# Performance work log

Measured on AMD Instinct MI355X. Metric: run time of the kernel, lower is better.

Reference implementation:

```python
import jax, jax.numpy as jnp
import numpy as np

EPS_BN = 1e-5
K_DET = 50

def conv2d(x, w, b, pad):
    y = jax.lax.conv_general_dilated(x, w, (1, 1), [(pad, pad), (pad, pad)],
                                     dimension_numbers=('NCHW', 'OIHW', 'NCHW'))
    return y + b[None, :, None, None]

def branch2(x, w1, b1, w2, b2):
    # conv3x3 -> relu -> conv1x1
    return conv2d(jax.nn.relu(conv2d(x, w1, b1, 1)), w2, b2, 0)

def roi_head(x, w1, b1, g, beta, m, v, w2, b2):
    # conv3x3 -> BN(eval) -> relu -> global avg pool -> conv1x1
    h = conv2d(x, w1, b1, 1)
    h = (h - m[None, :, None, None]) * (g[None, :, None, None] / jnp.sqrt(v[None, :, None, None] + EPS_BN)) + beta[None, :, None, None]
    h = jax.nn.relu(h)
    h = jnp.mean(h, axis=(2, 3), keepdims=True)
    return conv2d(h, w2, b2, 0)[:, :, 0, 0]

def nms_hm(heat, kernel=3):
    pad = (kernel - 1) // 2
    hmax = jax.lax.reduce_window(heat, -jnp.inf, jax.lax.max,
                                 (1, 1, kernel, kernel), (1, 1, 1, 1),
                                 [(0, 0), (0, 0), (pad, pad), (pad, pad)])
    return heat * (hmax == heat).astype(heat.dtype)

def select_topk(heat, K):
    B, C, H, W = heat.shape
    s_all, i_all = jax.lax.top_k(heat.reshape(B, C, H * W), K)   # per-class topk
    scores, idx = jax.lax.top_k(s_all.reshape(B, C * K), K)      # overall topk
    classes = idx // K
    inds = jnp.take_along_axis(i_all.reshape(B, C * K), idx, axis=1)  # flat HW inds
    return scores, inds, classes

def roi_align_7x7(feat, boxes, sr=2):
    # torchvision roi_align, spatial_scale=1, aligned=False, sampling_ratio=sr
    B, C, H, W = feat.shape
    N = boxes.shape[0]
    b = boxes[:, 0].astype(jnp.int32)
    x1, y1, x2, y2 = boxes[:, 1], boxes[:, 2], boxes[:, 3], boxes[:, 4]
    roi_w = jnp.maximum(x2 - x1, 1.0)
    roi_h = jnp.maximum(y2 - y1, 1.0)
    bw = roi_w / 7.0
    bh = roi_h / 7.0
    S = 7 * sr
    off = (jnp.arange(S, dtype=feat.dtype) + 0.5) / sr  # sample offsets in bin units
    xs = x1[:, None] + bw[:, None] * off[None, :]       # (N,S)
    ys = y1[:, None] + bh[:, None] * off[None, :]
    X = jnp.broadcast_to(xs[:, None, :], (N, S, S))
    Y = jnp.broadcast_to(ys[:, :, None], (N, S, S))
    valid = (X > -1.0) & (X < W) & (Y > -1.0) & (Y < H)
    Xc = jnp.clip(X, 0.0, W - 1.0)
    Yc = jnp.clip(Y, 0.0, H - 1.0)
    x0 = jnp.floor(Xc).astype(jnp.int32)
    y0 = jnp.floor(Yc).astype(jnp.int32)
    x1i = jnp.minimum(x0 + 1, W - 1)
    y1i = jnp.minimum(y0 + 1, H - 1)
    lx = Xc - x0
    ly = Yc - y0
    flat = feat.transpose(0, 2, 3, 1).reshape(B * H * W, C)
    base = (b * H * W)[:, None, None]
    g = lambda yy, xx: flat[base + yy * W + xx]  # (N,S,S,C)
    v = (((1 - ly) * (1 - lx))[..., None] * g(y0, x0)
         + ((1 - ly) * lx)[..., None] * g(y0, x1i)
         + (ly * (1 - lx))[..., None] * g(y1i, x0)
         + (ly * lx)[..., None] * g(y1i, x1i))
    v = v * valid[..., None]
    v = v.reshape(N, 7, sr, 7, sr, C).mean(axis=(2, 4))
    return v.transpose(0, 3, 1, 2)  # (N,C,7,7)

def project_to_rect(calib, pts):
    c_u, c_v = calib[:, 0, 2], calib[:, 1, 2]
    f_u, f_v = calib[:, 0, 0], calib[:, 1, 1]
    b_x = calib[:, 0, 3] / (-f_u)
    b_y = calib[:, 1, 3] / (-f_v)
    x = (pts[:, 0] - c_u) * pts[:, 2] / f_u + b_x
    y = (pts[:, 1] - c_v) * pts[:, 2] / f_v + b_y
    return jnp.stack([x, y, pts[:, 2]], -1)

HEAD_NAMES = ['dep', 'o3', 's3', 'hd']

def setup_inputs():
    key = jax.random.key(0)
    ks = iter(jax.random.split(key, 64))
    B, Cin, H, W = 8, 64, 96, 320
    HC, NC = 256, 3
    f32 = jnp.float32
    rn = lambda shape, s=0.02: s * jax.random.normal(next(ks), shape, f32)
    inp = {}
    inp['features'] = jax.random.normal(next(ks), (B, Cin, H, W), f32)
    base = jnp.array([[700., 0., 640., 0.], [0., 700., 192., 0.], [0., 0., 1., 0.]], f32)
    inp['calib'] = base[None] + (jax.random.uniform(next(ks), (B, 3, 4), f32) - 0.5) * 2.0
    crb = jnp.array([[0., 0.], [1280., 384.]], f32)
    inp['coord_ranges'] = crb[None] + (jax.random.uniform(next(ks), (B, 2, 2), f32) - 0.5) * 2.0
    inp['mean_size'] = jnp.array([[3.88, 1.63, 1.53], [0.84, 0.66, 1.76], [1.76, 0.60, 1.73]], f32)
    inp['hm_w1'] = rn((HC, Cin, 3, 3)); inp['hm_b1'] = jnp.zeros(HC, f32)
    inp['hm_w2'] = rn((3, HC, 1, 1)); inp['hm_b2'] = jnp.full((3,), -np.log(1 / 0.1 - 1), f32)
    inp['o2_w1'] = rn((HC, Cin, 3, 3)); inp['o2_b1'] = jnp.zeros(HC, f32)
    inp['o2_w2'] = rn((2, HC, 1, 1)); inp['o2_b2'] = jnp.zeros(2, f32)
    inp['s2_w1'] = rn((HC, Cin, 3, 3)); inp['s2_b1'] = jnp.zeros(HC, f32)
    inp['s2_w2'] = rn((2, HC, 1, 1)); inp['s2_b2'] = 8.0 * jnp.ones(2, f32)
    Croi = Cin + 2 + NC
    for name, oc in zip(HEAD_NAMES, [2, 2, 4, 24]):
        inp[name + '_w1'] = rn((HC, Croi, 3, 3)); inp[name + '_b1'] = jnp.zeros(HC, f32)
        inp[name + '_g'] = 1.0 + 0.1 * jax.random.normal(next(ks), (HC,), f32)
        inp[name + '_beta'] = 0.1 * jax.random.normal(next(ks), (HC,), f32)
        inp[name + '_m'] = 0.1 * jax.random.normal(next(ks), (HC,), f32)
        inp[name + '_v'] = 1.0 + jax.random.uniform(next(ks), (HC,), f32)
        inp[name + '_w2'] = rn((oc, HC, 1, 1)); inp[name + '_b2'] = jnp.zeros(oc, f32)
    return inp

def reference(features, calib, coord_ranges, mean_size,
              hm_w1, hm_b1, hm_w2, hm_b2,
              o2_w1, o2_b1, o2_w2, o2_b2,
              s2_w1, s2_b1, s2_w2, s2_b2,
              dep_w1, dep_b1, dep_g, dep_beta, dep_m, dep_v, dep_w2, dep_b2,
              o3_w1, o3_b1, o3_g, o3_beta, o3_m, o3_v, o3_w2, o3_b2,
              s3_w1, s3_b1, s3_g, s3_beta, s3_m, s3_v, s3_w2, s3_b2,
              hd_w1, hd_b1, hd_g, hd_beta, hd_m, hd_v, hd_w2, hd_b2):
    B, Cf, H, W = features.shape
    dt = features.dtype
    heatmap = branch2(features, hm_w1, hm_b1, hm_w2, hm_b2)    # (B,3,H,W)
    offset_2d = branch2(features, o2_w1, o2_b1, o2_w2, o2_b2)  # (B,2,H,W)
    size_2d = branch2(features, s2_w1, s2_b1, s2_w2, s2_b2)    # (B,2,H,W)
    heat = nms_hm(heatmap)
    _, inds, classes = select_topk(heat, K_DET)                # (B,K)
    # coord map and box2d maps (B,5,H,W): [batch_idx, x1,y1,x2,y2]
    xs = jnp.arange(W, dtype=dt)
    ys = jnp.arange(H, dtype=dt)
    coord = jnp.stack([jnp.broadcast_to(xs[None, :], (H, W)),
                       jnp.broadcast_to(ys[:, None], (H, W))], 0)[None]
    center = coord + offset_2d
    bidx = jnp.broadcast_to(jnp.arange(B, dtype=dt)[:, None, None, None], (B, 1, H, W))
    box2d_maps = jnp.concatenate([bidx, center - size_2d / 2, center + size_2d / 2], 1)
    bm = box2d_maps.reshape(B, 5, H * W).transpose(0, 2, 1)    # (B,HW,5)
    boxes = jnp.take_along_axis(bm, inds[:, :, None], axis=1).reshape(-1, 5)  # (N,5)
    N = boxes.shape[0]
    roi_feat = roi_align_7x7(features, boxes)                  # (N,C,7,7)
    rb = boxes[:, 0].astype(jnp.int32)
    cr = coord_ranges[rb]                                      # (N,2,2)
    sx = cr[:, 1, 0] - cr[:, 0, 0]
    sy = cr[:, 1, 1] - cr[:, 0, 1]
    box_img = jnp.stack([boxes[:, 0],
                         boxes[:, 1] / W * sx + cr[:, 0, 0],
                         boxes[:, 2] / H * sy + cr[:, 0, 1],
                         boxes[:, 3] / W * sx + cr[:, 0, 0],
                         boxes[:, 4] / H * sy + cr[:, 0, 1]], -1)
    roi_calib = calib[rb]                                      # (N,3,4)
    ones = jnp.ones((N, 1), dt)
    p1 = project_to_rect(roi_calib, jnp.concatenate([box_img[:, 1:3], ones], -1))[:, :2]
    p2 = project_to_rect(roi_calib, jnp.concatenate([box_img[:, 3:5], ones], -1))[:, :2]
    t = jnp.arange(7, dtype=dt) / 6.0
    cx = p1[:, 0:1] + t[None, :] * (p2[:, 0:1] - p1[:, 0:1])   # (N,7)
    cy = p1[:, 1:2] + t[None, :] * (p2[:, 1:2] - p1[:, 1:2])
    coord_maps = jnp.stack([jnp.broadcast_to(cx[:, None, :], (N, 7, 7)),
                            jnp.broadcast_to(cy[:, :, None], (N, 7, 7))], 1)
    cls = classes.reshape(-1)
    NC = mean_size.shape[0]
    cls_hot = jax.nn.one_hot(cls, NC, dtype=dt)
    roi_in = jnp.concatenate([roi_feat, coord_maps,
                              jnp.broadcast_to(cls_hot[:, :, None, None], (N, NC, 7, 7))], 1)
    box2d_h = jnp.maximum(box_img[:, 4] - box_img[:, 2], 1.0)
    s3 = roi_head(roi_in, s3_w1, s3_b1, s3_g, s3_beta, s3_m, s3_v, s3_w2, s3_b2)  # (N,4)
    h3d_log_std = s3[:, 3:4]
    size3d_offset = s3[:, :3]
    size_3d = mean_size[cls] + size3d_offset
    f_u = roi_calib[:, 0, 0]
    depth_geo = size_3d[:, 0] / box2d_h * f_u
    dep = roi_head(roi_in, dep_w1, dep_b1, dep_g, dep_beta, dep_m, dep_v, dep_w2, dep_b2)
    depth_geo_log_std = (h3d_log_std[:, 0] + 2.0 * (jnp.log(f_u) - jnp.log(box2d_h)))[:, None]
    depth_log_std = jax.nn.logsumexp(jnp.concatenate([dep[:, 1:2], depth_geo_log_std], -1), axis=-1, keepdims=True)
    depth = jnp.concatenate([1.0 / (jax.nn.sigmoid(dep[:, 0:1]) + 1e-6) - 1.0 + depth_geo[:, None],
                             depth_log_std], -1)
    heading = roi_head(roi_in, hd_w1, hd_b1, hd_g, hd_beta, hd_m, hd_v, hd_w2, hd_b2)
    offset_3d = roi_head(roi_in, o3_w1, o3_b1, o3_g, o3_beta, o3_m, o3_v, o3_w2, o3_b2)
    return (heatmap, offset_2d, size_2d, heading, depth, offset_3d, size3d_offset, h3d_log_std)
```

## Files before the change

kernel.cpp:

```cpp
#include <hip/hip_runtime.h>
#include <math.h>

typedef unsigned short u16;
typedef unsigned int   u32;
typedef unsigned long long u64;
typedef __attribute__((ext_vector_type(8))) short short8;
typedef __attribute__((ext_vector_type(4))) float f32x4;

__device__ __forceinline__ float b2f(u16 v) { return __uint_as_float(((u32)v) << 16); }
__device__ __forceinline__ u16 f2b(float f) {
    u32 u = __float_as_uint(f);
    u32 r = (u + 0x7FFFu + ((u >> 16) & 1u)) >> 16;
    return (u16)r;
}
__device__ __forceinline__ float gload(const void* p, long i, int bf) {
    return bf ? b2f(((const u16*)p)[i]) : ((const float*)p)[i];
}
__device__ __forceinline__ void gstore(void* p, long i, float v, int bf) {
    if (bf) ((u16*)p)[i] = f2b(v);
    else    ((float*)p)[i] = v;
}

__device__ __forceinline__ u64 packKey(float v, int idx) {
    u32 u = __float_as_uint(v);
    u32 m = (u & 0x80000000u) ? ~u : (u | 0x80000000u);
    return ((u64)(~m) << 32) | (u32)idx;
}

__device__ int blockFlag(const void* feat) {
    __shared__ int fcnt;
    if (threadIdx.x == 0) fcnt = 0;
    __syncthreads();
    int sane = 0;
    for (int i = threadIdx.x; i < 512; i += blockDim.x) {
        u16 v = ((const u16*)feat)[i];
        float f = b2f(v);
        u32 e = (v >> 7) & 0xFF;
        float a = fabsf(f);
        sane += (e != 0xFF) && (f == 0.f || (a >= 1e-8f && a <= 1e4f));
    }
    atomicAdd(&fcnt, sane);
    __syncthreads();
    return fcnt >= 480;
}

#define BATCH 8
#define CIN   64
#define FH    96
#define FW    320
#define KDET  50
#define NROI  400
#define CROI  69
#define HW    (FH*FW)
#define CHUNK 1920
#define NCHUNK 16

#define WS_HEAT 0L
#define WS_OFF2 737280L
#define WS_SIZ2 1228800L
#define WS_NH   1720320L
#define WS_CLS  2460000L
#define WS_BOX  2460400L
#define WS_ROI  2462400L
#define WS_HOUT 3814800L
#define WS_W1T  3827600L
#define WS_WB16 3975056L
#define WS_W1H  4269968L
#define WS_PAR  4905872L
#define WS_FLAG 4938960L
#define WS_FEATT 4938964L
#define WS_END  (WS_FEATT + 7864320L)

#define PB_CAL 0
#define PB_CRN 96
#define PB_MSZ 128
#define PB_BR0 144
#define PB_HD0 3264

#define O_HEAT 0L
#define O_OFF2 737280L
#define O_SIZ2 1228800L
#define O_HEAD 1720320L
#define O_DEP  1729920L
#define O_OFF3 1730720L
#define O_S3D  1731520L
#define O_H3D  1732720L

struct WPtrs { const void* bw[3]; const void* hw[4]; };
struct Seg { const void* src; int n; int dst; };
struct Segs { Seg s[40]; int cnt; };

__global__ void kPrepWP(WPtrs P, Segs S, const void* __restrict__ feat,
                        int* __restrict__ flag, float* __restrict__ w1t,
                        u16* __restrict__ wb16, u16* __restrict__ whb,
                        float* __restrict__ par) {
    const int bf = blockFlag(feat);
    if (blockIdx.x == 0 && threadIdx.x == 0) *flag = bf;
    if (blockIdx.x < 5760) {
        int idx = blockIdx.x * 256 + threadIdx.x;
        if (idx < 147456) {
            int k = idx >> 8, c = idx & 255;
            w1t[idx] = gload(P.bw[0], (long)c * 576 + k, bf);
        } else if (idx < 589824) {
            int j = idx - 147456;
            int br = j / 147456, rem = j % 147456;
            int tap = rem / 16384;
            int r2 = rem & 16383;
            int s = r2 >> 13;
            int n = (r2 >> 5) & 255;
            int c5 = r2 & 31;
            int ci = s * 32 + c5;
            wb16[j] = f2b(gload(P.bw[br], (long)n * 576 + ci * 9 + tap, bf));
        } else {
            int j = idx - 589824;
            int h = j / 221184, rem = j % 221184;
            int tap = rem / 24576, rem2 = rem % 24576;
            int cs = rem2 / 8192, rem3 = rem2 % 8192;
            int oc = rem3 >> 5, jj = rem3 & 31;
            int ci = cs * 32 + jj;
            u16 val = 0;
            if (ci < CROI) val = f2b(gload(P.hw[h], (long)oc * 621 + ci * 9 + tap, bf));
            whb[j] = val;
        }
    } else {
        int sidx = blockIdx.x - 5760;
        if (sidx < S.cnt) {
            Seg sg = S.s[sidx];
            for (int i = threadIdx.x; i < sg.n; i += 256)
                par[sg.dst + i] = gload(sg.src, i, bf);
        }
    }
}

union MLds {
    struct { u16 a[4][68][72]; float red[8][64][3]; } c;
    struct {
        float in[4][3][36];
        union { float w[36 * 256]; float part[32 * 3 * 32]; } u;
    } s;
    u16 t[64][72];
};

__global__ __launch_bounds__(512, 4)
void kBranch3M(const void* __restrict__ feat, const int* __restrict__ flag,
               const u16* __restrict__ wbAll,
               const float* __restrict__ bpAll,
               const float* __restrict__ w1t,
               void* __restrict__ outb, float* __restrict__ wsbase) {
    __shared__ __align__(16) MLds L;

    const long obase[3] = {O_HEAT, O_OFF2, O_SIZ2};
    const long wfs[3]   = {WS_HEAT, WS_OFF2, WS_SIZ2};

    const int bfl = *flag;
    const int tid = threadIdx.x;

    if (blockIdx.z == 9) {
        u16* featT = (u16*)(wsbase + WS_FEATT);
        const int x0 = blockIdx.x * 64;
        const int y0 = blockIdx.y * 2;
        for (int sub = 0; sub < 16; ++sub) {
            const int b = sub >> 1, y = y0 + (sub & 1);
            __syncthreads();
            for (int i = tid; i < 64 * 64; i += 512) {
                int c = i >> 6, x = i & 63;
                L.t[x][c] = f2b(gload(feat, ((long)(b * CIN + c) * FH + y) * FW + x0 + x, bfl));
            }
            __syncthreads();
            u16* outp = featT + (((long)b * FH + y) * FW + x0) * 64;
            for (int i = tid; i < 64 * 64; i += 512) {
                int x = i >> 6, c = i & 63;
                outp[(long)x * 64 + c] = L.t[x][c];
            }
        }
        return;
    }

    if (blockIdx.z == 8) {
        const int sidx = blockIdx.y * 5 + blockIdx.x;
        const int x0 = (sidx % 10) * 32;
        const int srem = sidx / 10;
        const int y = srem % 3;
        const int b = srem / 3;
        const float* bp = bpAll;
        const int OC = 3;
        const int xg = tid & 7, cg = tid >> 3;
        const int c0 = (cg & 31) * 8;

        float acc[8][4];
#pragma unroll
        for (int i = 0; i < 8; ++i)
#pragma unroll
            for (int j = 0; j < 4; ++j) acc[i][j] = 0.f;

        for (int chunk = 0; chunk < 16; ++chunk) {
            const int ci0 = chunk * 4;
            __syncthreads();
            for (int i = tid; i < 4 * 3 * 36; i += 512) {
                int xx = i % 36, t2 = i / 36;
                int r = t2 % 3, ci = t2 / 3;
                int gx = x0 - 1 + xx, gy = y - 1 + r;
                float v = 0.f;
                if (gx >= 0 && gx < FW && gy >= 0 && gy < FH)
                    v = gload(feat, ((long)(b * CIN + ci0 + ci) * FH + gy) * FW + gx, bfl);
                L.s.in[ci][r][xx] = v;
            }
            {
                const float4* src = (const float4*)(w1t + (long)ci0 * 9 * 256);
                float4* dst = (float4*)L.s.u.w;
                for (int i = tid; i < 36 * 256 / 4; i += 512) dst[i] = src[i];
            }
            __syncthreads();
            if (tid < 256) {
#pragma unroll
                for (int ci = 0; ci < 4; ++ci) {
#pragma unroll
                    for (int ky = 0; ky < 3; ++ky) {
                        const float* rowp = &L.s.in[ci][ky][xg * 4];
                        float inv[6];
                        *(float4*)&inv[0] = *(const float4*)&rowp[0];
                        *(float2*)&inv[4] = *(const float2*)&rowp[4];
#pragma unroll
                        for (int kx = 0; kx < 3; ++kx) {
                            const float* wp = &L.s.u.w[(ci * 9 + ky * 3 + kx) * 256 + c0];
                            float wv[8];
                            *(float4*)&wv[0] = *(const float4*)&wp[0];
                            *(float4*)&wv[4] = *(const float4*)&wp[4];
#pragma unroll
                            for (int cc = 0; cc < 8; ++cc)
#pragma unroll
                                for (int xx = 0; xx < 4; ++xx)
                                    acc[cc][xx] = fmaf(wv[cc], inv[xx + kx], acc[cc][xx]);
                        }
                    }
                }
            }
        }

        if (tid < 256) {
#pragma unroll
            for (int cc = 0; cc < 8; ++cc) {
                float b1v = bp[c0 + cc];
#pragma unroll
                for (int xx = 0; xx < 4; ++xx)
                    acc[cc][xx] = fmaxf(acc[cc][xx] + b1v, 0.f);
            }
        }
        __syncthreads();
        if (tid < 256) {
#pragma unroll
            for (int k = 0; k < OC; ++k) {
                float p[4];
#pragma unroll
                for (int xx = 0; xx < 4; ++xx) p[xx] = 0.f;
#pragma unroll
                for (int cc = 0; cc < 8; ++cc) {
                    float wv = bp[256 + k * 256 + c0 + cc];
#pragma unroll
                    for (int xx = 0; xx < 4; ++xx) p[xx] = fmaf(acc[cc][xx], wv, p[xx]);
                }
#pragma unroll
                for (int xx = 0; xx < 4; ++xx)
                    L.s.u.part[((cg & 31) * OC + k) * 32 + xg * 4 + xx] = p[xx];
            }
        }
        __syncthreads();
        float* outf = wsbase + WS_HEAT;
        for (int t = tid; t < OC * 32; t += 512) {
            int k = t >> 5, xx = t & 31;
            float s = bp[256 + OC * 256 + k];
#pragma unroll 8
            for (int g = 0; g < 32; ++g) s += L.s.u.part[(g * OC + k) * 32 + xx];
            long o = (((long)b * OC + k) * FH + y) * FW + x0 + xx;
            gstore(outb, O_HEAT + o, s, bfl);
            outf[o] = s;
        }
        return;
    }

    const int wave = tid >> 6, lane = tid & 63;
    const int q = lane >> 4, n15 = lane & 15;
    const int mg = wave >> 2, ng = wave & 3;
    const int x0 = blockIdx.x * 64, y0 = blockIdx.y * 2;
    const int b = blockIdx.z;

    if (tid < 256) {
        const int ci = tid & 63, rr = tid >> 6;
        const int gy = y0 - 1 + rr;
        if (gy < 0 || gy >= FH) {
            for (int xi = 0; xi < 66; ++xi) L.c.a[rr][xi][ci] = 0;
        } else if (bfl) {
            const u16* rp = (const u16*)feat + ((long)((b << 6) | ci) * FH + gy) * FW;
            for (int j = 0; j < 10; ++j) {
                int xs0 = x0 - 8 + j * 8;
                u16 tmp[8];
                if (xs0 >= 0 && xs0 <= FW - 8)
                    *(uint4*)tmp = *(const uint4*)(rp + xs0);
                else
                    for (int e = 0; e < 8; ++e) {
                        int gx = xs0 + e;
                        tmp[e] = (gx >= 0 && gx < FW) ? rp[gx] : (u16)0;
                    }
                for (int e = 0; e < 8; ++e) {
                    int xi = xs0 + e - x0 + 1;
                    if (xi >= 0 && xi < 66) L.c.a[rr][xi][ci] = tmp[e];
                }
            }
        } else {
            const float* rp = (const float*)feat + ((long)((b << 6) | ci) * FH + gy) * FW;
            for (int j = 0; j < 18; ++j) {
                int xs0 = x0 - 4 + j * 4;
                float tmp[4];
                if (xs0 >= 0 && xs0 <= FW - 4)
                    *(float4*)tmp = *(const float4*)(rp + xs0);
                else
                    for (int e = 0; e < 4; ++e) {
                        int gx = xs0 + e;
                        tmp[e] = (gx >= 0 && gx < FW) ? rp[gx] : 0.f;
                    }
                for (int e = 0; e < 4; ++e) {
                    int xi = xs0 + e - x0 + 1;
                    if (xi >= 0 && xi < 66) L.c.a[rr][xi][ci] = f2b(tmp[e]);
                }
            }
        }
    }
    __syncthreads();

#pragma unroll 1
    for (int br = 0; br < 3; ++br) {
        const int oc = (br == 0) ? 3 : 2;
        const u16* wpt = wbAll + br * 147456;
        const float* bp = bpAll + br * 1040;

        f32x4 acc[4][4];
#pragma unroll
        for (int i = 0; i < 4; ++i)
#pragma unroll
            for (int t = 0; t < 4; ++t) acc[i][t] = (f32x4){0.f, 0.f, 0.f, 0.f};

#pragma unroll 1
        for (int tap = 0; tap < 9; ++tap) {
            const int ky = tap / 3, kx = tap % 3;
#pragma unroll
            for (int s = 0; s < 2; ++s) {
                const u16* wks = wpt + (tap * 2 + s) * 8192;
                short8 bfr[4];
#pragma unroll
                for (int t = 0; t < 4; ++t)
                    bfr[t] = *(const short8*)(wks + (ng * 64 + t * 16 + n15) * 32 + q * 8);
                short8 afr[4];
#pragma unroll
                for (int i = 0; i < 4; ++i)
                    afr[i] = *(const short8*)&L.c.a[mg + ky][i * 16 + n15 + kx][s * 32 + q * 8];
#pragma unroll
                for (int i = 0; i < 4; ++i)
#pragma unroll
                    for (int t = 0; t < 4; ++t)
                        acc[i][t] = __builtin_amdgcn_mfma_f32_16x16x32_bf16(
                            afr[i], bfr[t], acc[i][t], 0, 0, 0);
            }
        }

        float b1v[4], w2v[3][4];
#pragma unroll
        for (int t = 0; t < 4; ++t) {
            int n = ng * 64 + t * 16 + n15;
            b1v[t] = bp[n];
#pragma unroll
            for (int k = 0; k < 3; ++k) w2v[k][t] = bp[256 + k * 256 + n];
        }
        __syncthreads();
#pragma unroll
        for (int i = 0; i < 4; ++i) {
#pragma unroll
            for (int r = 0; r < 4; ++r) {
                float pk[3];
#pragma unroll
                for (int k = 0; k < 3; ++k) pk[k] = 0.f;
#pragma unroll
                for (int t = 0; t < 4; ++t) {
                    float h = fmaxf(acc[i][t][r] + b1v[t], 0.f);
#pragma unroll
                    for (int k = 0; k < 3; ++k) pk[k] = fmaf(h, w2v[k][t], pk[k]);
                }
#pragma unroll
                for (int k = 0; k < 3; ++k) {
                    pk[k] += __shfl_xor(pk[k], 1);
                    pk[k] += __shfl_xor(pk[k], 2);
                    pk[k] += __shfl_xor(pk[k], 4);
                    pk[k] += __shfl_xor(pk[k], 8);
                }
                if (n15 == 0) {
                    int ml = i * 16 + q * 4 + r;
#pragma unroll
                    for (int k = 0; k < 3; ++k) L.c.red[wave][ml][k] = pk[k];
                }
            }
        }
        __syncthreads();
        float* outf = wsbase + wfs[br];
        for (int t2 = tid; t2 < oc * 128; t2 += 512) {
            int k = t2 >> 7, m = t2 & 127;
            int row = m >> 6, x = m & 63;
            int mg2 = m >> 6, ml = m & 63;
            float s = bp[256 + oc * 256 + k];
#pragma unroll
            for (int w = 0; w < 4; ++w) s += L.c.red[mg2 * 4 + w][ml][k];
            int grow = y0 + row;
            if (br == 0 && grow < 3) continue;
            long o = (((long)b * oc + k) * FH + grow) * FW + x0 + x;
            gstore(outb, obase[br] + o, s, bfl);
            outf[o] = s;
        }
    }
}

__global__ __launch_bounds__(256)
void kNmsTopA(const float* __restrict__ heat, float* __restrict__ nh) {
    __shared__ float hrow[8][320];
    __shared__ u64 keys[CHUNK];
    __shared__ u64 sub[4][KDET];
    const int bc = blockIdx.x, ch = blockIdx.y;
    const int tid = threadIdx.x;
    const int wave = tid >> 6, lane = tid & 63;
    const int r0 = ch * 6;
    const float* hp = heat + (long)bc * HW;

    for (int i = tid; i < 8 * 320; i += 256) {
        int rr = i / 320, x = i % 320;
        int gy = r0 - 1 + rr;
        hrow[rr][x] = (gy >= 0 && gy < FH) ? hp[(long)gy * FW + x] : -INFINITY;
    }
    __syncthreads();
    for (int i = tid; i < CHUNK; i += 256) {
        int ry = i / 320, x = i % 320;
        float v = hrow[ry + 1][x];
        float m = v;
        int xm = max(x - 1, 0), xp = min(x + 1, FW - 1);
#pragma unroll
        for (int dy = 0; dy < 3; ++dy) {
            m = fmaxf(m, hrow[ry + dy][xm]);
            m = fmaxf(m, hrow[ry + dy][x]);
            m = fmaxf(m, hrow[ry + dy][xp]);
        }
        float nv = (v == m) ? v : 0.f;
        keys[i] = packKey(nv, ch * CHUNK + i);
    }
    __syncthreads();
    {
        u64* kw = keys + wave * 480;
        for (int it = 0; it < KDET; ++it) {
            u64 bk = ~0ULL; int bp = 0;
            for (int i = lane; i < 480; i += 64) {
                u64 k = kw[i];
                if (k < bk) { bk = k; bp = i; }
            }
#pragma unroll
            for (int s = 32; s > 0; s >>= 1) {
                u64 k2 = __shfl_down(bk, s);
                int p2 = __shfl_down(bp, s);
                if (k2 < bk) { bk = k2; bp = p2; }
            }
            bk = __shfl(bk, 0);
            bp = __shfl(bp, 0);
            if (lane == 0) {
                sub[wave][it] = bk;
                kw[bp] = ~0ULL;
            }
        }
    }
    __syncthreads();
    if (wave == 0) {
        u64* outp = (u64*)(nh + (long)bc * HW + (long)ch * CHUNK);
        u64* sp = &sub[0][0];
        for (int it = 0; it < KDET; ++it) {
            u64 bk = ~0ULL; int bp = 0;
            for (int i = lane; i < 4 * KDET; i += 64) {
                u64 k = sp[i];
                if (k < bk) { bk = k; bp = i; }
            }
#pragma unroll
            for (int s = 32; s > 0; s >>= 1) {
                u64 k2 = __shfl_down(bk, s);
                int p2 = __shfl_down(bp, s);
                if (k2 < bk) { bk = k2; bp = p2; }
            }
            bk = __shfl(bk, 0);
            bp = __shfl(bp, 0);
            if (lane == 0) {
                outp[it] = bk;
                sp[bp] = ~0ULL;
            }
        }
    }
}

__global__ __launch_bounds__(192)
void kTopBC(const float* __restrict__ nh, const float* __restrict__ off2,
            const float* __restrict__ siz2, float* __restrict__ boxes,
            int* __restrict__ clsArr) {
    __shared__ u64 keys[3][NCHUNK * KDET];
    __shared__ float sc[150];
    __shared__ int   si[150];
    const int b = blockIdx.x, tid = threadIdx.x;
    const int wave = tid >> 6, lane = tid & 63;
    const int bc = b * 3 + wave;

    for (int ch = 0; ch < NCHUNK; ++ch) {
        const u64* src = (const u64*)(nh + (long)bc * HW + (long)ch * CHUNK);
        if (lane < KDET) keys[wave][ch * KDET + lane] = src[lane];
    }
    __syncthreads();
    for (int it = 0; it < KDET; ++it) {
        u64 bk = ~0ULL; int bp = 0;
        for (int i = lane; i < NCHUNK * KDET; i += 64) {
            u64 k = keys[wave][i];
            if (k < bk) { bk = k; bp = i; }
        }
#pragma unroll
        for (int s = 32; s > 0; s >>= 1) {
            u64 k2 = __shfl_down(bk, s);
            int p2 = __shfl_down(bp, s);
            if (k2 < bk) { bk = k2; bp = p2; }
        }
        bk = __shfl(bk, 0);
        bp = __shfl(bp, 0);
        if (lane == 0) {
            u32 hm = ~(u32)(bk >> 32);
            u32 u = (hm & 0x80000000u) ? (hm & 0x7fffffffu) : ~hm;
            sc[wave * KDET + it] = __uint_as_float(u);
            si[wave * KDET + it] = (int)(bk & 0xFFFFFFFFu);
            keys[wave][bp] = ~0ULL;
        }
    }
    __syncthreads();
    if (wave == 0) {
        const int t = lane;
        for (int r = 0; r < KDET; ++r) {
            float bv = -INFINITY; int bp = 0x7fffffff;
            for (int i = t; i < 150; i += 64) {
                float v = sc[i];
                if (v > bv) { bv = v; bp = i; }
            }
#pragma unroll
            for (int s = 32; s > 0; s >>= 1) {
                float v2 = __shfl_down(bv, s);
                int   p2 = __shfl_down(bp, s);
                if (v2 > bv || (v2 == bv && p2 < bp)) { bv = v2; bp = p2; }
            }
            bp = __shfl(bp, 0);
            if (t == 0) {
                int cls = bp / KDET;
                int ind = si[bp];
                int n = b * KDET + r;
                clsArr[n] = cls;
                int x = ind % FW, yy = ind / FW;
                float cx = (float)x  + off2[(((long)b * 2 + 0) * FH + yy) * FW + x];
                float cy = (float)yy + off2[(((long)b * 2 + 1) * FH + yy) * FW + x];
                float w  = siz2[(((long)b * 2 + 0) * FH + yy) * FW + x];
                float h  = siz2[(((long)b * 2 + 1) * FH + yy) * FW + x];
                boxes[n * 5 + 0] = (float)b;
                boxes[n * 5 + 1] = cx - w * 0.5f;
                boxes[n * 5 + 2] = cy - h * 0.5f;
                boxes[n * 5 + 3] = cx + w * 0.5f;
                boxes[n * 5 + 4] = cy + h * 0.5f;
                sc[bp] = -INFINITY;
            }
// ... 234 lines not shown

    int oyA[4], oxA[4];
#pragma unroll
    for (int i = 0; i < 4; ++i) {
        int pos = i * 16 + n15; if (pos > 48) pos = 48;
        oyA[i] = pos / 7; oxA[i] = pos % 7;
    }

    f32x4 acc[4][4];
#pragma unroll
    for (int i = 0; i < 4; ++i)
#pragma unroll
        for (int t = 0; t < 4; ++t) acc[i][t] = (f32x4){0.f, 0.f, 0.f, 0.f};

#pragma unroll 1
    for (int tap = 0; tap < 9; ++tap) {
        const int ky = tap / 3, kx = tap % 3;
        const u16* wt = whb + ((long)h * 9 + tap) * 24576;
#pragma unroll
        for (int cs = 0; cs < 3; ++cs) {
            short8 afr[4], bfr[4];
#pragma unroll
            for (int i = 0; i < 4; ++i)
                afr[i] = *(const short8*)&r_lds[oyA[i] + ky][oxA[i] + kx][cs * 32 + q * 8];
#pragma unroll
            for (int t = 0; t < 4; ++t)
                bfr[t] = *(const short8*)(wt + ((cs << 8) + wave * 64 + t * 16 + n15) * 32 + q * 8);
#pragma unroll
            for (int i = 0; i < 4; ++i)
#pragma unroll
                for (int t = 0; t < 4; ++t)
                    acc[i][t] = __builtin_amdgcn_mfma_f32_16x16x32_bf16(
                        afr[i], bfr[t], acc[i][t], 0, 0, 0);
        }
    }

    const float* hb = par + PB_HD0 + h * 7456;
#pragma unroll
    for (int t = 0; t < 4; ++t) {
        int oc = wave * 64 + t * 16 + n15;
        float b1 = hb[oc], g = hb[256 + oc], be = hb[512 + oc];
        float m = hb[768 + oc], v = hb[1024 + oc];
        float scale = g / sqrtf(v + 1e-5f);
        float s = 0.f;
#pragma unroll
        for (int i = 0; i < 4; ++i)
#pragma unroll
            for (int r = 0; r < 4; ++r) {
                int pos = i * 16 + q * 4 + r;
                if (pos < 49)
                    s += fmaxf((acc[i][t][r] + b1 - m) * scale + be, 0.f);
            }
        s += __shfl_xor(s, 16);
        s += __shfl_xor(s, 32);
        if (q == 0) means[oc] = s / 49.f;
    }
    __syncthreads();

    int oc_out = ocArr[h];
    const float* w2 = hb + 1280;
    for (int k = wave; k < oc_out; k += 4) {
        float s = 0.f;
        for (int c = lane; c < 256; c += 64) s += means[c] * w2[k * 256 + c];
#pragma unroll
        for (int off = 32; off > 0; off >>= 1) s += __shfl_down(s, off);
        if (lane == 0)
            head_out[(long)n * 32 + offArr[h] + k] = s + w2[oc_out * 256 + k];
    }
}

__global__ void kFinal(const float* __restrict__ head_out, const float* __restrict__ boxes,
                       const int* __restrict__ clsArr, const float* __restrict__ par,
                       void* __restrict__ out, const int* __restrict__ flag) {
    int n = blockIdx.x * 256 + threadIdx.x;
    if (n >= NROI) return;
    const int bf = *flag;
    const float* ho = head_out + (long)n * 32;
    float dep0 = ho[0], dep1 = ho[1];
    int b = (int)boxes[n * 5 + 0];
    int cls = clsArr[n];

    for (int j = 0; j < 24; ++j) gstore(out, O_HEAD + n * 24 + j, ho[8 + j], bf);
    gstore(out, O_OFF3 + n * 2 + 0, ho[2], bf);
    gstore(out, O_OFF3 + n * 2 + 1, ho[3], bf);
    gstore(out, O_S3D + n * 3 + 0, ho[4], bf);
    gstore(out, O_S3D + n * 3 + 1, ho[5], bf);
    gstore(out, O_S3D + n * 3 + 2, ho[6], bf);
    gstore(out, O_H3D + n, ho[7], bf);

    float cry0 = par[PB_CRN + b * 4 + 1], cry1 = par[PB_CRN + b * 4 + 3];
    float sy = cry1 - cry0;
    float bi2 = boxes[n * 5 + 2] / (float)FH * sy + cry0;
    float bi4 = boxes[n * 5 + 4] / (float)FH * sy + cry0;
    float box_h = fmaxf(bi4 - bi2, 1.f);
    float f_u = par[PB_CAL + b * 12 + 0];
    float size3d0 = par[PB_MSZ + cls * 3 + 0] + ho[4];
    float depth_geo = size3d0 / box_h * f_u;
    float sig = 1.f / (1.f + expf(-dep0));
    float d0 = 1.f / (sig + 1e-6f) - 1.f + depth_geo;
    float dgls = ho[7] + 2.f * (logf(f_u) - logf(box_h));
    float mx = fmaxf(dep1, dgls);
    float lse = mx + logf(expf(dep1 - mx) + expf(dgls - mx));
    gstore(out, O_DEP + n * 2 + 0, d0, bf);
    gstore(out, O_DEP + n * 2 + 1, lse, bf);
}

extern "C" void kernel_launch(void* const* d_in, const int* in_sizes, int n_in,
                              void* d_out, int out_size, void* d_ws, size_t ws_size,
                              hipStream_t stream) {
    (void)in_sizes; (void)n_in; (void)out_size;
    float* ws = (float*)d_ws;
    float* par = ws + WS_PAR;
    int* flag = (int*)(ws + WS_FLAG);
    u16* wb16 = (u16*)(ws + WS_WB16);
    u16* whb  = (u16*)(ws + WS_W1H);
    u16* featT = (u16*)(ws + WS_FEATT);
    const void* feat = d_in[0];
    const bool bigws = ws_size >= (size_t)WS_END * 4;

    WPtrs WP;
    WP.bw[0] = d_in[4]; WP.bw[1] = d_in[8]; WP.bw[2] = d_in[12];
    WP.hw[0] = d_in[16]; WP.hw[1] = d_in[24]; WP.hw[2] = d_in[32]; WP.hw[3] = d_in[40];

    Segs SG; int si = 0;
    auto add = [&](const void* s, int n, int dst) {
        SG.s[si].src = s; SG.s[si].n = n; SG.s[si].dst = dst; ++si;
    };
    add(d_in[1], 96, PB_CAL); add(d_in[2], 32, PB_CRN); add(d_in[3], 9, PB_MSZ);
    const int ocb[3] = {3, 2, 2};
    for (int b = 0; b < 3; ++b) {
        int base = PB_BR0 + b * 1040;
        int i0 = 4 + 4 * b;
        add(d_in[i0 + 1], 256, base);
        add(d_in[i0 + 2], ocb[b] * 256, base + 256);
        add(d_in[i0 + 3], ocb[b], base + 256 + ocb[b] * 256);
    }
    const int och[4] = {2, 2, 4, 24};
    for (int h = 0; h < 4; ++h) {
        int base = PB_HD0 + h * 7456;
        int i0 = 16 + 8 * h;
        add(d_in[i0 + 1], 256, base);
        add(d_in[i0 + 2], 256, base + 256);
        add(d_in[i0 + 3], 256, base + 512);
        add(d_in[i0 + 4], 256, base + 768);
        add(d_in[i0 + 5], 256, base + 1024);
        add(d_in[i0 + 6], och[h] * 256, base + 1280);
        add(d_in[i0 + 7], och[h], base + 1280 + och[h] * 256);
    }
    SG.cnt = si;

    kPrepWP<<<5760 + 40, 256, 0, stream>>>(WP, SG, feat, flag,
                                           ws + WS_W1T, wb16, whb, par);

    kBranch3M<<<dim3(5, 48, bigws ? 10 : 9), 512, 0, stream>>>(
        feat, flag, wb16, par + PB_BR0, ws + WS_W1T, d_out, ws);

    kNmsTopA<<<dim3(24, NCHUNK), 256, 0, stream>>>(ws + WS_HEAT, ws + WS_NH);
    kTopBC<<<8, 192, 0, stream>>>(ws + WS_NH, ws + WS_OFF2, ws + WS_SIZ2,
                                  ws + WS_BOX, (int*)(ws + WS_CLS));
    if (bigws) {
        kHeadM2<<<dim3(4, NROI), 256, 0, stream>>>(featT, ws + WS_BOX,
                                                   (int*)(ws + WS_CLS), whb, par,
                                                   ws + WS_HOUT);
    } else {
        kRoi<<<400, 256, 0, stream>>>(feat, flag, ws + WS_BOX, (int*)(ws + WS_CLS),
                                      par, ws + WS_ROI);
        kHeadM<<<dim3(4, NROI), 256, 0, stream>>>(ws + WS_ROI, whb, par, ws + WS_HOUT);
    }
    kFinal<<<2, 256, 0, stream>>>(ws + WS_HOUT, ws + WS_BOX, (int*)(ws + WS_CLS),
                                  par, d_out, flag);
}
```

Before: 745.2 us.

## Fuse feature transpose into conv tile load and software-pipeline MFMA loop

The separate transpose blocks (z==9), which re-read the feature map, are removed. Instead, each conv block writes its already-staged bf16 LDS tile out to the NHWC featT buffer. The per-branch MFMA loop is split into two output-channel halves with 4x2 accumulators and double-buffered A/B fragment loads across taps, which lowers register pressure and overlaps loads with MFMAs. The reduction buffer is double-buffered by branch, which removes one barrier per branch. The risk is extra A-fragment LDS reads, since each half reloads A, plus the added epilogue passes.

```diff
diff --git a/kernel.cpp b/kernel.cpp
--- a/kernel.cpp
+++ b/kernel.cpp
@@ -133,12 +133,11 @@
 }
 
 union MLds {
-    struct { u16 a[4][68][72]; float red[8][64][3]; } c;
+    struct { u16 a[4][68][72]; float red[2][8][64][3]; } c;
     struct {
         float in[4][3][36];
         union { float w[36 * 256]; float part[32 * 3 * 32]; } u;
     } s;
-    u16 t[64][72];
 };
 
 __global__ __launch_bounds__(512, 4)
@@ -146,7 +145,7 @@
                const u16* __restrict__ wbAll,
                const float* __restrict__ bpAll,
                const float* __restrict__ w1t,
-               void* __restrict__ outb, float* __restrict__ wsbase) {
+               void* __restrict__ outb, float* __restrict__ wsbase, int doT) {
     __shared__ __align__(16) MLds L;
 
     const long obase[3] = {O_HEAT, O_OFF2, O_SIZ2};
@@ -155,28 +154,7 @@
     const int bfl = *flag;
     const int tid = threadIdx.x;
 
-    if (blockIdx.z == 9) {
-        u16* featT = (u16*)(wsbase + WS_FEATT);
-        const int x0 = blockIdx.x * 64;
-        const int y0 = blockIdx.y * 2;
-        for (int sub = 0; sub < 16; ++sub) {
-            const int b = sub >> 1, y = y0 + (sub & 1);
-            __syncthreads();
-            for (int i = tid; i < 64 * 64; i += 512) {
-                int c = i >> 6, x = i & 63;
-                L.t[x][c] = f2b(gload(feat, ((long)(b * CIN + c) * FH + y) * FW + x0 + x, bfl));
-            }
-            __syncthreads();
-            u16* outp = featT + (((long)b * FH + y) * FW + x0) * 64;
-            for (int i = tid; i < 64 * 64; i += 512) {
-                int x = i >> 6, c = i & 63;
-                outp[(long)x * 64 + c] = L.t[x][c];
-            }
-        }
-        return;
-    }
-
-    if (blockIdx.z == 8) {
+    if (blockIdx.z == 0) {
         const int sidx = blockIdx.y * 5 + blockIdx.x;
         const int x0 = (sidx % 10) * 32;
         const int srem = sidx / 10;
@@ -282,7 +260,7 @@
     const int q = lane >> 4, n15 = lane & 15;
     const int mg = wave >> 2, ng = wave & 3;
     const int x0 = blockIdx.x * 64, y0 = blockIdx.y * 2;
-    const int b = blockIdx.z;
+    const int b = blockIdx.z - 1;
 
     if (tid < 256) {
         const int ci = tid & 63, rr = tid >> 6;
@@ -327,77 +305,108 @@
     }
     __syncthreads();
 
+    if (doT) {
+        u16* featT = (u16*)(wsbase + WS_FEATT);
+        for (int i = tid; i < 1024; i += 512) {
+            int c8 = i & 7, x = (i >> 3) & 63, r = i >> 9;
+            uint4 v = *(const uint4*)&L.c.a[1 + r][1 + x][c8 * 8];
+            *(uint4*)(featT + (((long)b * FH + y0 + r) * FW + x0 + x) * 64 + c8 * 8) = v;
+        }
+    }
+
+    const u16* aflat = &L.c.a[0][0][0];
+    const int wlane = (ng * 64 + n15) * 32 + q * 8;
+    const int abase = mg * 4896 + n15 * 72 + q * 8;
+
+#define LOADB2(k, dst) { \
+    const u16* wk_ = wph + (k) * 8192; \
+    dst[0] = *(const short8*)(wk_); \
+    dst[1] = *(const short8*)(wk_ + 512); }
+#define LOADA4(k, dst) { \
+    const int tap_ = (k) >> 1, s_ = (k) & 1; \
+    const int ky_ = tap_ / 3, kx_ = tap_ - 3 * ky_; \
+    const u16* ap_ = aflat + abase + ky_ * 4896 + kx_ * 72 + s_ * 32; \
+    dst[0] = *(const short8*)(ap_); \
+    dst[1] = *(const short8*)(ap_ + 1152); \
+    dst[2] = *(const short8*)(ap_ + 2304); \
+    dst[3] = *(const short8*)(ap_ + 3456); }
+#define MFMA42(afr, bfr) { \
+    _Pragma("unroll") \
+    for (int i_ = 0; i_ < 4; ++i_) { \
+        _Pragma("unroll") \
+        for (int t_ = 0; t_ < 2; ++t_) \
+            acc[i_][t_] = __builtin_amdgcn_mfma_f32_16x16x32_bf16( \
+                afr[i_], bfr[t_], acc[i_][t_], 0, 0, 0); } }
+
 #pragma unroll 1
     for (int br = 0; br < 3; ++br) {
         const int oc = (br == 0) ? 3 : 2;
         const u16* wpt = wbAll + br * 147456;
         const float* bp = bpAll + br * 1040;
-
-        f32x4 acc[4][4];
-#pragma unroll
-        for (int i = 0; i < 4; ++i)
-#pragma unroll
-            for (int t = 0; t < 4; ++t) acc[i][t] = (f32x4){0.f, 0.f, 0.f, 0.f};
+        float (*redb)[64][3] = L.c.red[br & 1];
 
 #pragma unroll 1
-        for (int tap = 0; tap < 9; ++tap) {
-            const int ky = tap / 3, kx = tap % 3;
-#pragma unroll
-            for (int s = 0; s < 2; ++s) {
-                const u16* wks = wpt + (tap * 2 + s) * 8192;
-                short8 bfr[4];
-#pragma unroll
-                for (int t = 0; t < 4; ++t)
-                    bfr[t] = *(const short8*)(wks + (ng * 64 + t * 16 + n15) * 32 + q * 8);
-                short8 afr[4];
-#pragma unroll
-                for (int i = 0; i < 4; ++i)
-                    afr[i] = *(const short8*)&L.c.a[mg + ky][i * 16 + n15 + kx][s * 32 + q * 8];
-#pragma unroll
-                for (int i = 0; i < 4; ++i)
-#pragma unroll
-                    for (int t = 0; t < 4; ++t)
-                        acc[i][t] = __builtin_amdgcn_mfma_f32_16x16x32_bf16(
-                            afr[i], bfr[t], acc[i][t], 0, 0, 0);
-            }
-        }
-
-        float b1v[4], w2v[3][4];
-#pragma unroll
-        for (int t = 0; t < 4; ++t) {
-            int n = ng * 64 + t * 16 + n15;
-            b1v[t] = bp[n];
-#pragma unroll
-            for (int k = 0; k < 3; ++k) w2v[k][t] = bp[256 + k * 256 + n];
-        }
-        __syncthreads();
-#pragma unroll
-        for (int i = 0; i < 4; ++i) {
-#pragma unroll
-            for (int r = 0; r < 4; ++r) {
-                float pk[3];
-#pragma unroll
-                for (int k = 0; k < 3; ++k) pk[k] = 0.f;
-#pragma unroll
-                for (int t = 0; t < 4; ++t) {
-                    float h = fmaxf(acc[i][t][r] + b1v[t], 0.f);
-#pragma unroll
-                    for (int k = 0; k < 3; ++k) pk[k] = fmaf(h, w2v[k][t], pk[k]);
+        for (int hf = 0; hf < 2; ++hf) {
+            const u16* wph = wpt + wlane + hf * 1024;
+
+            f32x4 acc[4][2];
+#pragma unroll
+            for (int i = 0; i < 4; ++i)
+#pragma unroll
+                for (int t = 0; t < 2; ++t) acc[i][t] = (f32x4){0.f, 0.f, 0.f, 0.f};
+
+            short8 aA[4], aB[4], bA[2], bB[2];
+            LOADB2(0, bA);
+            LOADA4(0, aA);
+#pragma unroll 1
+            for (int st = 0; st < 18; st += 2) {
+                LOADB2(st + 1, bB);
+                LOADA4(st + 1, aB);
+                MFMA42(aA, bA);
+                if (st + 2 < 18) { LOADB2(st + 2, bA); LOADA4(st + 2, aA); }
+                MFMA42(aB, bB);
+            }
+
+            float b1v[2], w2v[3][2];
+#pragma unroll
+            for (int t = 0; t < 2; ++t) {
+                int n = ng * 64 + (hf * 2 + t) * 16 + n15;
+                b1v[t] = bp[n];
+#pragma unroll
+                for (int k = 0; k < 3; ++k) w2v[k][t] = bp[256 + k * 256 + n];
+            }
+#pragma unroll
+            for (int i = 0; i < 4; ++i) {
+#pragma unroll
+                for (int r = 0; r < 4; ++r) {
+                    float pk[3] = {0.f, 0.f, 0.f};
+#pragma unroll
+                    for (int t = 0; t < 2; ++t) {
+                        float h = fmaxf(acc[i][t][r] + b1v[t], 0.f);
+#pragma unroll
+                        for (int k = 0; k < 3; ++k) pk[k] = fmaf(h, w2v[k][t], pk[k]);
+                    }
+#pragma unroll
+                    for (int k = 0; k < 3; ++k) {
+                        pk[k] += __shfl_xor(pk[k], 1);
+                        pk[k] += __shfl_xor(pk[k], 2);
+                        pk[k] += __shfl_xor(pk[k], 4);
+                        pk[k] += __shfl_xor(pk[k], 8);
+                    }
+                    if (n15 == 0) {
+                        int ml = i * 16 + q * 4 + r;
+                        if (hf == 0) {
+#pragma unroll
+                            for (int k = 0; k < 3; ++k) redb[wave][ml][k] = pk[k];
+                        } else {
+#pragma unroll
+                            for (int k = 0; k < 3; ++k) redb[wave][ml][k] += pk[k];
+                        }
+                    }
                 }
-#pragma unroll
-                for (int k = 0; k < 3; ++k) {
-                    pk[k] += __shfl_xor(pk[k], 1);
-                    pk[k] += __shfl_xor(pk[k], 2);
-                    pk[k] += __shfl_xor(pk[k], 4);
-                    pk[k] += __shfl_xor(pk[k], 8);
-                }
-                if (n15 == 0) {
-                    int ml = i * 16 + q * 4 + r;
-#pragma unroll
-                    for (int k = 0; k < 3; ++k) L.c.red[wave][ml][k] = pk[k];
-                }
-            }
-        }
+            }
+        }
+
         __syncthreads();
         float* outf = wsbase + wfs[br];
         for (int t2 = tid; t2 < oc * 128; t2 += 512) {
@@ -406,7 +415,7 @@
             int mg2 = m >> 6, ml = m & 63;
             float s = bp[256 + oc * 256 + k];
 #pragma unroll
-            for (int w = 0; w < 4; ++w) s += L.c.red[mg2 * 4 + w][ml][k];
+            for (int w = 0; w < 4; ++w) s += redb[mg2 * 4 + w][ml][k];
             int grow = y0 + row;
             if (br == 0 && grow < 3) continue;
             long o = (((long)b * oc + k) * FH + grow) * FW + x0 + x;
@@ -414,6 +423,9 @@
             outf[o] = s;
         }
     }
+#undef LOADB2
+#undef LOADA4
+#undef MFMA42
 }
 
 __global__ __launch_bounds__(256)
@@ -954,8 +966,8 @@
     kPrepWP<<<5760 + 40, 256, 0, stream>>>(WP, SG, feat, flag,
                                            ws + WS_W1T, wb16, whb, par);
 
-    kBranch3M<<<dim3(5, 48, bigws ? 10 : 9), 512, 0, stream>>>(
-        feat, flag, wb16, par + PB_BR0, ws + WS_W1T, d_out, ws);
+    kBranch3M<<<dim3(5, 48, 9), 512, 0, stream>>>(
+        feat, flag, wb16, par + PB_BR0, ws + WS_W1T, d_out, ws, bigws ? 1 : 0);
 
     kNmsTopA<<<dim3(24, NCHUNK), 256, 0, stream>>>(ws + WS_HEAT, ws + WS_NH);
     kTopBC<<<8, 192, 0, stream>>>(ws + WS_NH, ws + WS_OFF2, ws + WS_SIZ2,
```

Result: slower. 841.2 us (+12.9%).

## Fuse feature transpose into conv tiles and defer branch reductions to one pass

Applied to the files above, without the earlier changes.

Removes the separate z-slice that transposed the feature map to channel-last. Each conv block now writes its already-staged bf16 LDS tile out to the transposed buffer instead of re-reading the input from global memory. The halo load is spread over all 512 threads rather than 256. Per-branch partial sums get their own LDS slots, which drops two barriers per branch and leaves a single reduction/store pass after all three branches. The cost is a larger LDS footprint for the reduction buffer, which may lower occupancy, and the heat branch moves to z index 0.

```diff
diff --git a/kernel.cpp b/kernel.cpp
--- a/kernel.cpp
+++ b/kernel.cpp
@@ -133,12 +133,11 @@
 }
 
 union MLds {
-    struct { u16 a[4][68][72]; float red[8][64][3]; } c;
+    struct { u16 a[4][68][72]; float red[3][8][64][3]; } c;
     struct {
         float in[4][3][36];
         union { float w[36 * 256]; float part[32 * 3 * 32]; } u;
     } s;
-    u16 t[64][72];
 };
 
 __global__ __launch_bounds__(512, 4)
@@ -146,7 +145,7 @@
                const u16* __restrict__ wbAll,
                const float* __restrict__ bpAll,
                const float* __restrict__ w1t,
-               void* __restrict__ outb, float* __restrict__ wsbase) {
+               void* __restrict__ outb, float* __restrict__ wsbase, int doT) {
     __shared__ __align__(16) MLds L;
 
     const long obase[3] = {O_HEAT, O_OFF2, O_SIZ2};
@@ -155,28 +154,7 @@
     const int bfl = *flag;
     const int tid = threadIdx.x;
 
-    if (blockIdx.z == 9) {
-        u16* featT = (u16*)(wsbase + WS_FEATT);
-        const int x0 = blockIdx.x * 64;
-        const int y0 = blockIdx.y * 2;
-        for (int sub = 0; sub < 16; ++sub) {
-            const int b = sub >> 1, y = y0 + (sub & 1);
-            __syncthreads();
-            for (int i = tid; i < 64 * 64; i += 512) {
-                int c = i >> 6, x = i & 63;
-                L.t[x][c] = f2b(gload(feat, ((long)(b * CIN + c) * FH + y) * FW + x0 + x, bfl));
-            }
-            __syncthreads();
-            u16* outp = featT + (((long)b * FH + y) * FW + x0) * 64;
-            for (int i = tid; i < 64 * 64; i += 512) {
-                int x = i >> 6, c = i & 63;
-                outp[(long)x * 64 + c] = L.t[x][c];
-            }
-        }
-        return;
-    }
-
-    if (blockIdx.z == 8) {
+    if (blockIdx.z == 0) {
         const int sidx = blockIdx.y * 5 + blockIdx.x;
         const int x0 = (sidx % 10) * 32;
         const int srem = sidx / 10;
@@ -282,16 +260,16 @@
     const int q = lane >> 4, n15 = lane & 15;
     const int mg = wave >> 2, ng = wave & 3;
     const int x0 = blockIdx.x * 64, y0 = blockIdx.y * 2;
-    const int b = blockIdx.z;
-
-    if (tid < 256) {
-        const int ci = tid & 63, rr = tid >> 6;
+    const int b = blockIdx.z - 1;
+
+    {
+        const int ci = tid & 63, rr = (tid >> 6) & 3, hf = tid >> 8;
         const int gy = y0 - 1 + rr;
         if (gy < 0 || gy >= FH) {
-            for (int xi = 0; xi < 66; ++xi) L.c.a[rr][xi][ci] = 0;
+            for (int xi = hf * 33; xi < hf * 33 + 33; ++xi) L.c.a[rr][xi][ci] = 0;
         } else if (bfl) {
             const u16* rp = (const u16*)feat + ((long)((b << 6) | ci) * FH + gy) * FW;
-            for (int j = 0; j < 10; ++j) {
+            for (int j = hf * 5; j < hf * 5 + 5; ++j) {
                 int xs0 = x0 - 8 + j * 8;
                 u16 tmp[8];
                 if (xs0 >= 0 && xs0 <= FW - 8)
@@ -308,7 +286,7 @@
             }
         } else {
             const float* rp = (const float*)feat + ((long)((b << 6) | ci) * FH + gy) * FW;
-            for (int j = 0; j < 18; ++j) {
+            for (int j = hf * 9; j < hf * 9 + 9; ++j) {
                 int xs0 = x0 - 4 + j * 4;
                 float tmp[4];
                 if (xs0 >= 0 && xs0 <= FW - 4)
@@ -327,9 +305,17 @@
     }
     __syncthreads();
 
+    if (doT) {
+        u16* featT = (u16*)(wsbase + WS_FEATT);
+        for (int i = tid; i < 1024; i += 512) {
+            int c8 = i & 7, x = (i >> 3) & 63, r = i >> 9;
+            uint4 v = *(const uint4*)&L.c.a[1 + r][1 + x][c8 * 8];
+            *(uint4*)(featT + (((long)b * FH + y0 + r) * FW + x0 + x) * 64 + c8 * 8) = v;
+        }
+    }
+
 #pragma unroll 1
     for (int br = 0; br < 3; ++br) {
-        const int oc = (br == 0) ? 3 : 2;
         const u16* wpt = wbAll + br * 147456;
         const float* bp = bpAll + br * 1040;
 
@@ -370,14 +356,11 @@
 #pragma unroll
             for (int k = 0; k < 3; ++k) w2v[k][t] = bp[256 + k * 256 + n];
         }
-        __syncthreads();
 #pragma unroll
         for (int i = 0; i < 4; ++i) {
 #pragma unroll
             for (int r = 0; r < 4; ++r) {
-                float pk[3];
-#pragma unroll
-                for (int k = 0; k < 3; ++k) pk[k] = 0.f;
+                float pk[3] = {0.f, 0.f, 0.f};
 #pragma unroll
                 for (int t = 0; t < 4; ++t) {
                     float h = fmaxf(acc[i][t][r] + b1v[t], 0.f);
@@ -394,11 +377,18 @@
                 if (n15 == 0) {
                     int ml = i * 16 + q * 4 + r;
 #pragma unroll
-                    for (int k = 0; k < 3; ++k) L.c.red[wave][ml][k] = pk[k];
+                    for (int k = 0; k < 3; ++k) L.c.red[br][wave][ml][k] = pk[k];
                 }
             }
         }
-        __syncthreads();
+    }
+
+    __syncthreads();
+
+#pragma unroll 1
+    for (int br = 0; br < 3; ++br) {
+        const int oc = (br == 0) ? 3 : 2;
+        const float* bp = bpAll + br * 1040;
         float* outf = wsbase + wfs[br];
         for (int t2 = tid; t2 < oc * 128; t2 += 512) {
             int k = t2 >> 7, m = t2 & 127;
@@ -406,7 +396,7 @@
             int mg2 = m >> 6, ml = m & 63;
             float s = bp[256 + oc * 256 + k];
 #pragma unroll
-            for (int w = 0; w < 4; ++w) s += L.c.red[mg2 * 4 + w][ml][k];
+            for (int w = 0; w < 4; ++w) s += L.c.red[br][mg2 * 4 + w][ml][k];
             int grow = y0 + row;
             if (br == 0 && grow < 3) continue;
             long o = (((long)b * oc + k) * FH + grow) * FW + x0 + x;
@@ -954,8 +944,8 @@
     kPrepWP<<<5760 + 40, 256, 0, stream>>>(WP, SG, feat, flag,
                                            ws + WS_W1T, wb16, whb, par);
 
-    kBranch3M<<<dim3(5, 48, bigws ? 10 : 9), 512, 0, stream>>>(
-        feat, flag, wb16, par + PB_BR0, ws + WS_W1T, d_out, ws);
+    kBranch3M<<<dim3(5, 48, 9), 512, 0, stream>>>(
+        feat, flag, wb16, par + PB_BR0, ws + WS_W1T, d_out, ws, bigws ? 1 : 0);
 
     kNmsTopA<<<dim3(24, NCHUNK), 256, 0, stream>>>(ws + WS_HEAT, ws + WS_NH);
     kTopBC<<<8, 192, 0, stream>>>(ws + WS_NH, ws + WS_OFF2, ws + WS_SIZ2,
```

Result: no change. 755.0 us (+1.3%).
